# Kernel optimization log

Measured on AMD Instinct MI355X. Metric: run time of the kernel, lower is better.

## Reference

```python
import jax, jax.numpy as jnp
import numpy as np

EPS = 1e-5  # BatchNorm eps


def _add_self_loops(edge_index, num_nodes):
    loop = jnp.arange(num_nodes, dtype=edge_index.dtype)
    src = jnp.concatenate([edge_index[0], loop])
    dst = jnp.concatenate([edge_index[1], loop])
    return src, dst


def _gcn_conv(x, src, dst, norm, W, b, num_nodes):
    # PyG GCNConv: out = D^{-1/2} (A+I) D^{-1/2} (x W) + b
    h = x @ W                                # [N, out_dim]
    msg = h[src] * norm[:, None]             # [E+N, out_dim] gathered messages
    out = jax.ops.segment_sum(msg, dst, num_segments=num_nodes)
    return out + b


def _batch_norm(x, gamma, beta):
    # training-mode batch statistics over the node dimension (biased var)
    mean = jnp.mean(x, axis=0)
    var = jnp.var(x, axis=0)
    return (x - mean) * jax.lax.rsqrt(var + EPS) * gamma + beta


def setup_inputs() -> dict:
    key = jax.random.key(0)
    ks = jax.random.split(key, 10)
    N, E = 50000, 800000
    d_in, d_h, d_mid, d_out = 1536, 512, 128, 5

    x = jax.random.normal(ks[0], (N, d_in), dtype=jnp.float32)
    edge_index = jax.random.randint(ks[1], (2, E), 0, N, dtype=jnp.int32)

    def glorot(k, fan_in, fan_out):
        s = jnp.sqrt(6.0 / (fan_in + fan_out))
        return jax.random.uniform(k, (fan_in, fan_out), jnp.float32, -s, s)

    return {
        "x": x,
        "edge_index": edge_index,
        "W1": glorot(ks[2], d_in, d_h), "b1": jnp.zeros((d_h,), jnp.float32),
        "W2": glorot(ks[3], d_h, d_mid), "b2": jnp.zeros((d_mid,), jnp.float32),
        "W3": glorot(ks[4], d_mid, d_out), "b3": jnp.zeros((d_out,), jnp.float32),
        "gamma1": jnp.ones((d_h,), jnp.float32), "beta1": jnp.zeros((d_h,), jnp.float32),
        "gamma2": jnp.ones((d_mid,), jnp.float32), "beta2": jnp.zeros((d_mid,), jnp.float32),
    }


def reference(x, edge_index, W1, b1, W2, b2, W3, b3, gamma1, beta1, gamma2, beta2):
    N = x.shape[0]
    src, dst = _add_self_loops(edge_index, N)
    # symmetric degree normalization deg^{-1/2}[src] * deg^{-1/2}[dst]
    deg = jax.ops.segment_sum(jnp.ones_like(dst, dtype=x.dtype), dst, num_segments=N)
    inv_sqrt = jnp.where(deg > 0, jax.lax.rsqrt(deg), 0.0)
    norm = inv_sqrt[src] * inv_sqrt[dst]

    h = _gcn_conv(x, src, dst, norm, W1, b1, N)
    h = jax.nn.relu(_batch_norm(h, gamma1, beta1))  # dropout is identity in eval
    h = _gcn_conv(h, src, dst, norm, W2, b2, N)
    h = jax.nn.relu(_batch_norm(h, gamma2, beta2))
    h = _gcn_conv(h, src, dst, norm, W3, b3, N)
    return jax.nn.log_softmax(h, axis=1)
```

## Files before the change

### kernel.cpp

```cpp
#include <hip/hip_runtime.h>
#include <cstddef>
#include <cstdint>

typedef short s16x8 __attribute__((ext_vector_type(8)));
typedef unsigned short u16x4 __attribute__((ext_vector_type(4)));
typedef unsigned short u16x8 __attribute__((ext_vector_type(8)));
typedef float f32x4 __attribute__((ext_vector_type(4)));

__device__ __forceinline__ unsigned short f2bf(float f) {
  unsigned int u = __float_as_uint(f);
  u = (u + 0x7fffu + ((u >> 16) & 1u)) >> 16;
  return (unsigned short)u;
}
__device__ __forceinline__ float bf2f(unsigned short u) {
  return __uint_as_float(((unsigned int)u) << 16);
}

__device__ __forceinline__ void gl2lds16(const unsigned short* g, unsigned short* l) {
  __builtin_amdgcn_global_load_lds(
      (const __attribute__((address_space(1))) unsigned int*)g,
      (__attribute__((address_space(3))) unsigned int*)l, 16, 0, 0);
}

static inline size_t alignup(size_t x) { return (x + 255) & ~(size_t)255; }

__global__ void cvt_bf16_kernel(const float* __restrict__ in, unsigned short* __restrict__ out,
                                long n8) {
  long stride = (long)gridDim.x * blockDim.x;
  const float4* in4 = reinterpret_cast<const float4*>(in);
  u16x8* out8 = reinterpret_cast<u16x8*>(out);
  for (long i = blockIdx.x * (long)blockDim.x + threadIdx.x; i < n8; i += stride) {
    float4 a = in4[2 * i], b = in4[2 * i + 1];
    u16x8 p;
    p[0] = f2bf(a.x); p[1] = f2bf(a.y); p[2] = f2bf(a.z); p[3] = f2bf(a.w);
    p[4] = f2bf(b.x); p[5] = f2bf(b.y); p[6] = f2bf(b.z); p[7] = f2bf(b.w);
    out8[i] = p;
  }
}

__global__ void count_kernel(const int* __restrict__ dst, int* __restrict__ counts, int E) {
  int e = blockIdx.x * blockDim.x + threadIdx.x;
  if (e < E) atomicAdd(&counts[dst[e]], 1);
}

__global__ void invsqrt_kernel(const int* __restrict__ counts, float* __restrict__ inv_s, int n) {
  int i = blockIdx.x * blockDim.x + threadIdx.x;
  if (i < n) inv_s[i] = rsqrtf((float)(counts[i] + 1));
}

__global__ void block_sum_kernel(const int* __restrict__ counts, int* __restrict__ bsum, int n) {
  __shared__ int red[256];
  int i = blockIdx.x * 256 + threadIdx.x;
  red[threadIdx.x] = (i < n) ? counts[i] : 0;
  __syncthreads();
  #pragma unroll
  for (int o = 128; o > 0; o >>= 1) {
    if (threadIdx.x < o) red[threadIdx.x] += red[threadIdx.x + o];
    __syncthreads();
  }
  if (threadIdx.x == 0) bsum[blockIdx.x] = red[0];
}

__global__ void scan_bsum_kernel(int* __restrict__ bsum, int nb) {
  __shared__ int s[256];
  int t = threadIdx.x;
  s[t] = (t < nb) ? bsum[t] : 0;
  __syncthreads();
  #pragma unroll
  for (int o = 1; o < 256; o <<= 1) {
    int v = (t >= o) ? s[t - o] : 0;
    __syncthreads();
    s[t] += v;
    __syncthreads();
  }
  if (t < nb) bsum[t] = (t == 0) ? 0 : s[t - 1];
}

__global__ void scan_apply_kernel(const int* __restrict__ counts, const int* __restrict__ bpre,
                                  int* __restrict__ offsets, int n) {
  __shared__ int s[256];
  int t = threadIdx.x;
  int i = blockIdx.x * 256 + t;
  s[t] = (i < n) ? counts[i] : 0;
  __syncthreads();
  #pragma unroll
  for (int o = 1; o < 256; o <<= 1) {
    int v = (t >= o) ? s[t - o] : 0;
    __syncthreads();
    s[t] += v;
    __syncthreads();
  }
  if (i < n) offsets[i + 1] = s[t] + bpre[blockIdx.x];
  if (i == 0) offsets[0] = 0;
}

__global__ void fill_kernel(const int* __restrict__ src, const int* __restrict__ dst,
                            const int* __restrict__ offsets, int* __restrict__ cursor,
                            int* __restrict__ csr_src, int E) {
  int e = blockIdx.x * blockDim.x + threadIdx.x;
  if (e >= E) return;
  int d = dst[e];
  int pos = atomicAdd(&cursor[d], 1);
  csr_src[offsets[d] + pos] = src[e];
}

__global__ void transpose_w_kernel(const float* __restrict__ W, unsigned short* __restrict__ Wt,
                                   int K, int N) {
  __shared__ float tile[32][33];
  int k0 = blockIdx.x * 32, n0 = blockIdx.y * 32;
  int tx = threadIdx.x & 31, ty = threadIdx.x >> 5;
  #pragma unroll
  for (int i = 0; i < 32; i += 8)
    tile[ty + i][tx] = W[(size_t)(k0 + ty + i) * N + n0 + tx];
  __syncthreads();
  #pragma unroll
  for (int i = 0; i < 32; i += 8)
    Wt[(size_t)(n0 + ty + i) * K + k0 + tx] = f2bf(tile[tx][ty + i]);
}

__global__ __launch_bounds__(256) void gemm1_kernel(
    const unsigned short* __restrict__ A, const unsigned short* __restrict__ B,
    unsigned short* __restrict__ C, int M) {
  __shared__ __align__(16) unsigned short As[128 * 64];
  __shared__ __align__(16) unsigned short Bs[128 * 64];
  const int K = 1536;
  int tid = threadIdx.x, lane = tid & 63, w = tid >> 6;

  int nwg = gridDim.x * gridDim.y;
  int orig = blockIdx.y * gridDim.x + blockIdx.x;
  int q = nwg >> 3, r = nwg & 7;
  int xcd = orig & 7, loc = orig >> 3;
  int wg = (xcd < r) ? xcd * (q + 1) + loc : r * (q + 1) + (xcd - r) * q + loc;
  int bx = wg & 3, by = wg >> 2;

  int m0 = by * 128, n0 = bx * 128;
  int wm = (w >> 1) * 64, wn = (w & 1) * 64;

  f32x4 acc[4][4];
  #pragma unroll
  for (int i = 0; i < 4; i++)
    #pragma unroll
    for (int j = 0; j < 4; j++) acc[i][j] = (f32x4){0.f, 0.f, 0.f, 0.f};

  int srow[4], sgc[4];
  #pragma unroll
  for (int i = 0; i < 4; i++) {
    int s = i * 256 + tid;
    int row = s >> 3, j = s & 7;
    srow[i] = row;
    sgc[i] = (j ^ (row & 7)) << 3;
  }

  for (int k0 = 0; k0 < K; k0 += 64) {
    #pragma unroll
    for (int i = 0; i < 4; i++) {
      int s = i * 256 + tid;
      gl2lds16(&A[(size_t)(m0 + srow[i]) * K + k0 + sgc[i]], &As[s * 8]);
      gl2lds16(&B[(size_t)(n0 + srow[i]) * K + k0 + sgc[i]], &Bs[s * 8]);
    }
    __syncthreads();
    #pragma unroll
    for (int ks = 0; ks < 2; ks++) {
      s16x8 af[4], bfr[4];
      int jc = ks * 4 + (lane >> 4);
      #pragma unroll
      for (int i = 0; i < 4; i++) {
        int rr = wm + i * 16 + (lane & 15);
        af[i] = *reinterpret_cast<const s16x8*>(&As[rr * 64 + ((jc ^ (rr & 7)) << 3)]);
        int rn = wn + i * 16 + (lane & 15);
        bfr[i] = *reinterpret_cast<const s16x8*>(&Bs[rn * 64 + ((jc ^ (rn & 7)) << 3)]);
      }
      #pragma unroll
      for (int i = 0; i < 4; i++)
        #pragma unroll
        for (int j = 0; j < 4; j++)
          acc[i][j] = __builtin_amdgcn_mfma_f32_16x16x32_bf16(af[i], bfr[j], acc[i][j], 0, 0, 0);
    }
    __syncthreads();
  }
  #pragma unroll
  for (int i = 0; i < 4; i++) {
    #pragma unroll
    for (int j = 0; j < 4; j++) {
      int col = n0 + wn + j * 16 + (lane & 15);
      #pragma unroll
      for (int r2 = 0; r2 < 4; r2++) {
        int row = m0 + wm + i * 16 + (lane >> 4) * 4 + r2;
        if (row < M) C[(size_t)row * 512 + col] = f2bf(acc[i][j][r2]);
      }
    }
  }
}

#define LDT 72
__global__ __launch_bounds__(256) void gemm2_kernel(
    const unsigned short* __restrict__ A, const unsigned short* __restrict__ Bt,
    const float* __restrict__ sc, const float* __restrict__ sh,
    unsigned short* __restrict__ C, int M) {
  const int N = 128, K = 512;
  __shared__ unsigned short As[128 * LDT];
  __shared__ unsigned short Bs[128 * LDT];
  int tid = threadIdx.x;
  int m0 = blockIdx.y * 128;
  int w = tid >> 6, lane = tid & 63;
  int wm = (w >> 1) * 64, wn = (w & 1) * 64;

  f32x4 acc[4][4];
  #pragma unroll
  for (int i = 0; i < 4; i++)
    #pragma unroll
    for (int j = 0; j < 4; j++) acc[i][j] = (f32x4){0.f, 0.f, 0.f, 0.f};

  for (int k0 = 0; k0 < K; k0 += 64) {
    #pragma unroll
    for (int r = 0; r < 4; r++) {
      int idx = r * 256 + tid;
      int row = idx >> 3;
      int seg = (idx & 7) * 8;
      int gr = m0 + row;
      u16x8 v = (u16x8){0, 0, 0, 0, 0, 0, 0, 0};
      if (gr < M) v = *reinterpret_cast<const u16x8*>(&A[(size_t)gr * K + k0 + seg]);
      int c = k0 + seg;
      u16x8 p;
      #pragma unroll
      for (int j = 0; j < 8; j++) {
        float f = fmaxf(bf2f(v[j]) * sc[c + j] + sh[c + j], 0.f);
        p[j] = f2bf(f);
      }
      *reinterpret_cast<u16x8*>(&As[row * LDT + seg]) = p;
    }
    #pragma unroll
    for (int r = 0; r < 4; r++) {
      int idx = r * 256 + tid;
      int n = idx >> 3;
      int seg = (idx & 7) * 8;
      u16x8 v = *reinterpret_cast<const u16x8*>(&Bt[(size_t)n * K + k0 + seg]);
      *reinterpret_cast<u16x8*>(&Bs[n * LDT + seg]) = v;
    }
    __syncthreads();
    #pragma unroll
    for (int ks = 0; ks < 2; ks++) {
      s16x8 af[4], bfr[4];
      #pragma unroll
      for (int i = 0; i < 4; i++) {
        af[i]  = *reinterpret_cast<const s16x8*>(&As[(wm + i * 16 + (lane & 15)) * LDT + ks * 32 + (lane >> 4) * 8]);
        bfr[i] = *reinterpret_cast<const s16x8*>(&Bs[(wn + i * 16 + (lane & 15)) * LDT + ks * 32 + (lane >> 4) * 8]);
      }
      #pragma unroll
      for (int i = 0; i < 4; i++)
        #pragma unroll
        for (int j = 0; j < 4; j++)
          acc[i][j] = __builtin_amdgcn_mfma_f32_16x16x32_bf16(af[i], bfr[j], acc[i][j], 0, 0, 0);
    }
    __syncthreads();
  }
  #pragma unroll
  for (int i = 0; i < 4; i++) {
    #pragma unroll
    for (int j = 0; j < 4; j++) {
      int col = wn + j * 16 + (lane & 15);
      #pragma unroll
      for (int r = 0; r < 4; r++) {
        int row = m0 + wm + i * 16 + (lane >> 4) * 4 + r;
        if (row < M) C[(size_t)row * N + col] = f2bf(acc[i][j][r]);
      }
    }
  }
}

__global__ void agg512_kernel(const unsigned short* __restrict__ h, const int* __restrict__ offsets,
                              const int* __restrict__ csr, const float* __restrict__ inv_s,
                              unsigned short* __restrict__ out, int n) {
  int wv = threadIdx.x >> 6, lane = threadIdx.x & 63;
  int node = blockIdx.x * 4 + wv;
  if (node >= n) return;
  const u16x8* h8 = reinterpret_cast<const u16x8*>(h);
  float di = inv_s[node];
  size_t rb = (size_t)node * 64;
  float acc[8];
  u16x8 v0 = h8[rb + lane];
  float dd = di * di;
  #pragma unroll
  for (int j = 0; j < 8; j++) acc[j] = bf2f(v0[j]) * dd;
  int e = offsets[node], e1 = offsets[node + 1];
  for (; e + 1 < e1; e += 2) {
    int sA = csr[e], sB = csr[e + 1];
    float wA = inv_s[sA] * di, wB = inv_s[sB] * di;
    u16x8 vA = h8[(size_t)sA * 64 + lane];
    u16x8 vB = h8[(size_t)sB * 64 + lane];
    #pragma unroll
    for (int j = 0; j < 8; j++) acc[j] += bf2f(vA[j]) * wA + bf2f(vB[j]) * wB;
  }
  if (e < e1) {
    int sA = csr[e];
    float wA = inv_s[sA] * di;
    u16x8 vA = h8[(size_t)sA * 64 + lane];
    #pragma unroll
    for (int j = 0; j < 8; j++) acc[j] += bf2f(vA[j]) * wA;
  }
  u16x8 o;
  #pragma unroll
  for (int j = 0; j < 8; j++) o[j] = f2bf(acc[j]);
  reinterpret_cast<u16x8*>(out)[rb + lane] = o;
}

__global__ void agg128_kernel(const unsigned short* __restrict__ h, const int* __restrict__ offsets,
                              const int* __restrict__ csr, const float* __restrict__ inv_s,
                              unsigned short* __restrict__ out, int n) {
  int wv = threadIdx.x >> 6, lane = threadIdx.x & 63;
  int node = blockIdx.x * 4 + wv;
  if (node >= n) return;
  const unsigned int* h2 = reinterpret_cast<const unsigned int*>(h);
  float di = inv_s[node];
  size_t rb = (size_t)node * 64;
  unsigned int u0 = h2[rb + lane];
  float dd = di * di;
  float alo = __uint_as_float(u0 << 16) * dd;
  float ahi = __uint_as_float(u0 & 0xffff0000u) * dd;
  int e = offsets[node], e1 = offsets[node + 1];
  for (; e + 1 < e1; e += 2) {
    int sA = csr[e], sB = csr[e + 1];
    float wA = inv_s[sA] * di, wB = inv_s[sB] * di;
    unsigned int uA = h2[(size_t)sA * 64 + lane];
    unsigned int uB = h2[(size_t)sB * 64 + lane];
    alo += __uint_as_float(uA << 16) * wA + __uint_as_float(uB << 16) * wB;
    ahi += __uint_as_float(uA & 0xffff0000u) * wA + __uint_as_float(uB & 0xffff0000u) * wB;
  }
  if (e < e1) {
    int sA = csr[e];
    float wA = inv_s[sA] * di;
    unsigned int uA = h2[(size_t)sA * 64 + lane];
    alo += __uint_as_float(uA << 16) * wA;
    ahi += __uint_as_float(uA & 0xffff0000u) * wA;
  }
  unsigned int uo = ((unsigned int)f2bf(ahi) << 16) | (unsigned int)f2bf(alo);
  reinterpret_cast<unsigned int*>(out)[rb + lane] = uo;
}

__global__ void bn_stats512_kernel(const unsigned short* __restrict__ x, float* __restrict__ accum,
                                   int nrows, int rpb) {
  int r0 = blockIdx.x * rpb, r1 = min(nrows, r0 + rpb);
  int t = threadIdx.x;
  const unsigned int* x2 = reinterpret_cast<const unsigned int*>(x);
  float s0 = 0.f, q0 = 0.f, s1 = 0.f, q1 = 0.f;
  for (int r = r0; r < r1; r++) {
    unsigned int u = x2[(size_t)r * 256 + t];
    float lo = __uint_as_float(u << 16);
    float hi = __uint_as_float(u & 0xffff0000u);
    s0 += lo; q0 += lo * lo; s1 += hi; q1 += hi * hi;
  }
  atomicAdd(&accum[2 * t], s0);
  atomicAdd(&accum[2 * t + 1], s1);
  atomicAdd(&accum[512 + 2 * t], q0);
  atomicAdd(&accum[512 + 2 * t + 1], q1);
}

__global__ void bn_stats128_kernel(const unsigned short* __restrict__ x, float* __restrict__ accum,
                                   int nrows, int rpb) {
  int r0 = blockIdx.x * rpb, r1 = min(nrows, r0 + rpb);
  int t = threadIdx.x;
  int colu = t & 63, rofs = t >> 6;
  const unsigned int* x2 = reinterpret_cast<const unsigned int*>(x);
  float s0 = 0.f, q0 = 0.f, s1 = 0.f, q1 = 0.f;
  for (int r = r0 + rofs; r < r1; r += 4) {
    unsigned int u = x2[(size_t)r * 64 + colu];
    float lo = __uint_as_float(u << 16);
    float hi = __uint_as_float(u & 0xffff0000u);
    s0 += lo; q0 += lo * lo; s1 += hi; q1 += hi * hi;
  }
  atomicAdd(&accum[2 * colu], s0);
  atomicAdd(&accum[2 * colu + 1], s1);
  atomicAdd(&accum[128 + 2 * colu], q0);
  atomicAdd(&accum[128 + 2 * colu + 1], q1);
}

__global__ void bn_finalize_kernel(const float* __restrict__ accum, const float* __restrict__ gamma,
                                   const float* __restrict__ beta, float* __restrict__ scale,
                                   float* __restrict__ shift, int D, float invN) {
  int c = blockIdx.x * blockDim.x + threadIdx.x;
  if (c >= D) return;
  float mean = accum[c] * invN;
  float var = accum[D + c] * invN - mean * mean;
  float sc = gamma[c] * rsqrtf(var + 1e-5f);
  scale[c] = sc;
  shift[c] = beta[c] - mean * sc;
}

__global__ void gemm3_kernel(const unsigned short* __restrict__ A, const float* __restrict__ W,
                             const float* __restrict__ sc, const float* __restrict__ sh,
                             float* __restrict__ C, int M) {
  __shared__ float Ws[128 * 5];
  __shared__ float scs[128], shs[128];
  int tid = threadIdx.x;
  for (int i = tid; i < 128 * 5; i += blockDim.x) Ws[i] = W[i];
  if (tid < 128) { scs[tid] = sc[tid]; shs[tid] = sh[tid]; }
  __syncthreads();
  int row = blockIdx.x * blockDim.x + tid;
  if (row >= M) return;
  float acc[5] = {0.f, 0.f, 0.f, 0.f, 0.f};
  const u16x8* a8 = reinterpret_cast<const u16x8*>(A + (size_t)row * 128);
  for (int k8 = 0; k8 < 16; k8++) {
    u16x8 v = a8[k8];
    int k = k8 * 8;
    #pragma unroll
    for (int j = 0; j < 8; j++) {
      float f = fmaxf(bf2f(v[j]) * scs[k + j] + shs[k + j], 0.f);
      #pragma unroll
      for (int c = 0; c < 5; c++) acc[c] += f * Ws[(k + j) * 5 + c];
    }
  }
  #pragma unroll
  for (int j = 0; j < 5; j++) C[(size_t)row * 5 + j] = acc[j];
}

__global__ void agg3_lsm_kernel(const float* __restrict__ h, const int* __restrict__ offsets,
                                const int* __restrict__ csr, const float* __restrict__ inv_s,
                                const float* __restrict__ b3, float* __restrict__ out, int n) {
  int node = blockIdx.x * blockDim.x + threadIdx.x;
  if (node >= n) return;
  float di = inv_s[node];
  float acc[5];
  #pragma unroll
  for (int j = 0; j < 5; j++) acc[j] = h[(size_t)node * 5 + j] * di * di;
  int s0 = offsets[node], s1 = offsets[node + 1];
  for (int e = s0; e < s1; e++) {
    int s = csr[e];
    float wgt = inv_s[s] * di;
    #pragma unroll
    for (int j = 0; j < 5; j++) acc[j] += h[(size_t)s * 5 + j] * wgt;
  }
  #pragma unroll
  for (int j = 0; j < 5; j++) acc[j] += b3[j];
  float m = acc[0];
  #pragma unroll
  for (int j = 1; j < 5; j++) m = fmaxf(m, acc[j]);
  float sum = 0.f;
  #pragma unroll
  for (int j = 0; j < 5; j++) sum += expf(acc[j] - m);
  float lse = logf(sum);
  #pragma unroll
  for (int j = 0; j < 5; j++) out[(size_t)node * 5 + j] = acc[j] - m - lse;
}

extern "C" void kernel_launch(void* const* d_in, const int* in_sizes, int n_in,
                              void* d_out, int out_size, void* d_ws, size_t ws_size,
                              hipStream_t stream) {
  const float* x      = (const float*)d_in[0];
  const int*   ei     = (const int*)d_in[1];
  const float* W1     = (const float*)d_in[2];
  const float* b3     = (const float*)d_in[7];
  const float* W2     = (const float*)d_in[4];
  const float* W3     = (const float*)d_in[6];
  const float* gamma1 = (const float*)d_in[8];
  const float* beta1  = (const float*)d_in[9];
  const float* gamma2 = (const float*)d_in[10];
  const float* beta2  = (const float*)d_in[11];

  const int N = in_sizes[0] / 1536;
  const int E = in_sizes[1] / 2;
  const int* src = ei;
  const int* dst = ei + E;

  const int mblocks = (N + 127) / 128;
  const int Mpad = mblocks * 128;
  const int nb = (N + 255) / 256;

  char* ws = (char*)d_ws;
  size_t szRA = alignup((size_t)N * 512 * sizeof(float));
  size_t szXB = alignup((size_t)Mpad * 1536 * sizeof(unsigned short));
  char* RAb = ws;
  unsigned short* XB = (unsigned short*)(ws + szRA);
  char* RBb = ws + szRA;
  char* sp = ws + szRA + szXB;
  int* counts   = (int*)sp;           sp += alignup((size_t)N * 4);
  int* cursor   = (int*)sp;           sp += alignup((size_t)N * 4);
  int* offsets  = (int*)sp;           sp += alignup((size_t)(N + 1) * 4);
  int* csr_src  = (int*)sp;           sp += alignup((size_t)E * 4);
  float* inv_s  = (float*)sp;         sp += alignup((size_t)N * 4);
  unsigned short* W1t = (unsigned short*)sp; sp += alignup((size_t)512 * 1536 * 2);
  unsigned short* W2t = (unsigned short*)sp; sp += alignup((size_t)128 * 512 * 2);
  float* accum  = (float*)sp;         sp += alignup(1024 * 4);
  float* sc1    = (float*)sp;         sp += alignup(512 * 4);
  float* sh1    = (float*)sp;         sp += alignup(512 * 4);
  float* sc2    = (float*)sp;         sp += alignup(128 * 4);
  float* sh2    = (float*)sp;         sp += alignup(128 * 4);
  int* bsum     = (int*)sp;           sp += alignup(256 * 4);

  unsigned short* H1  = (unsigned short*)RAb;
  unsigned short* G1  = (unsigned short*)RBb;
  unsigned short* H2  = (unsigned short*)RAb;
  unsigned short* G2  = (unsigned short*)RBb;
  float*          H3  = (float*)RAb;

  cvt_bf16_kernel<<<2048, 256, 0, stream>>>(x, XB, (long)N * 1536 / 8);
  hipMemsetAsync(XB + (size_t)N * 1536, 0, (size_t)(Mpad - N) * 1536 * 2, stream);

  hipMemsetAsync(counts, 0, (size_t)N * 4, stream);
  hipMemsetAsync(cursor, 0, (size_t)N * 4, stream);
  count_kernel<<<(E + 255) / 256, 256, 0, stream>>>(dst, counts, E);
  invsqrt_kernel<<<(N + 255) / 256, 256, 0, stream>>>(counts, inv_s, N);
  block_sum_kernel<<<nb, 256, 0, stream>>>(counts, bsum, N);
  scan_bsum_kernel<<<1, 256, 0, stream>>>(bsum, nb);
  scan_apply_kernel<<<nb, 256, 0, stream>>>(counts, bsum, offsets, N);
  fill_kernel<<<(E + 255) / 256, 256, 0, stream>>>(src, dst, offsets, cursor, csr_src, E);

  transpose_w_kernel<<<dim3(1536 / 32, 512 / 32), 256, 0, stream>>>(W1, W1t, 1536, 512);
  transpose_w_kernel<<<dim3(512 / 32, 128 / 32), 256, 0, stream>>>(W2, W2t, 512, 128);

  int aggblocks = (N + 3) / 4;
  int rpb = (N + 511) / 512;

  gemm1_kernel<<<dim3(4, mblocks), 256, 0, stream>>>(XB, W1t, H1, N);
  agg512_kernel<<<aggblocks, 256, 0, stream>>>(H1, offsets, csr_src, inv_s, G1, N);
  hipMemsetAsync(accum, 0, 1024 * 4, stream);
  bn_stats512_kernel<<<512, 256, 0, stream>>>(G1, accum, N, rpb);
  bn_finalize_kernel<<<2, 256, 0, stream>>>(accum, gamma1, beta1, sc1, sh1, 512, 1.0f / N);

  gemm2_kernel<<<dim3(1, mblocks), 256, 0, stream>>>(G1, W2t, sc1, sh1, H2, N);
  agg128_kernel<<<aggblocks, 256, 0, stream>>>(H2, offsets, csr_src, inv_s, G2, N);
  hipMemsetAsync(accum, 0, 1024 * 4, stream);
  bn_stats128_kernel<<<512, 256, 0, stream>>>(G2, accum, N, rpb);
  bn_finalize_kernel<<<1, 256, 0, stream>>>(accum, gamma2, beta2, sc2, sh2, 128, 1.0f / N);

  gemm3_kernel<<<(N + 255) / 256, 256, 0, stream>>>(G2, W3, sc2, sh2, H3, N);
  agg3_lsm_kernel<<<(N + 255) / 256, 256, 0, stream>>>(H3, offsets, csr_src, inv_s, b3,
                                                       (float*)d_out, N);
}
```

Baseline: 695.5 us.

## Fuse fp32-to-bf16 conversion of x into GEMM1 A-tile loading

Removes the separate conversion kernel and padding memset for x. GEMM1 now reads fp32 x directly, converts it to bf16 in registers with packed convert instructions, and stores it into swizzled LDS. Out-of-range rows are zero-filled. This avoids writing and rereading a bf16 copy of x, but GEMM1 now reads twice as many bytes for A. Those loads are synchronous register loads rather than async global-to-LDS copies, and since gridDim.x is 4, each A row is converted four times.

```diff
diff --git a/kernel.cpp b/kernel.cpp
--- a/kernel.cpp
+++ b/kernel.cpp
@@ -23,20 +23,6 @@
 }
 
 static inline size_t alignup(size_t x) { return (x + 255) & ~(size_t)255; }
-
-__global__ void cvt_bf16_kernel(const float* __restrict__ in, unsigned short* __restrict__ out,
-                                long n8) {
-  long stride = (long)gridDim.x * blockDim.x;
-  const float4* in4 = reinterpret_cast<const float4*>(in);
-  u16x8* out8 = reinterpret_cast<u16x8*>(out);
-  for (long i = blockIdx.x * (long)blockDim.x + threadIdx.x; i < n8; i += stride) {
-    float4 a = in4[2 * i], b = in4[2 * i + 1];
-    u16x8 p;
-    p[0] = f2bf(a.x); p[1] = f2bf(a.y); p[2] = f2bf(a.z); p[3] = f2bf(a.w);
-    p[4] = f2bf(b.x); p[5] = f2bf(b.y); p[6] = f2bf(b.z); p[7] = f2bf(b.w);
-    out8[i] = p;
-  }
-}
 
 __global__ void count_kernel(const int* __restrict__ dst, int* __restrict__ counts, int E) {
   int e = blockIdx.x * blockDim.x + threadIdx.x;
@@ -119,7 +105,7 @@
 }
 
 __global__ __launch_bounds__(256) void gemm1_kernel(
-    const unsigned short* __restrict__ A, const unsigned short* __restrict__ B,
+    const float* __restrict__ A, const unsigned short* __restrict__ B,
     unsigned short* __restrict__ C, int M) {
   __shared__ __align__(16) unsigned short As[128 * 64];
   __shared__ __align__(16) unsigned short Bs[128 * 64];
@@ -142,20 +128,38 @@
     #pragma unroll
     for (int j = 0; j < 4; j++) acc[i][j] = (f32x4){0.f, 0.f, 0.f, 0.f};
 
-  int srow[4], sgc[4];
+  int srow[4], sgc[4], adst[4];
+  const float* aptr[4];
+  bool aok[4];
   #pragma unroll
   for (int i = 0; i < 4; i++) {
     int s = i * 256 + tid;
     int row = s >> 3, j = s & 7;
     srow[i] = row;
     sgc[i] = (j ^ (row & 7)) << 3;
+    adst[i] = row * 64 + sgc[i];
+    aok[i] = (m0 + row) < M;
+    aptr[i] = A + (size_t)(m0 + row) * K + j * 8;
   }
 
   for (int k0 = 0; k0 < K; k0 += 64) {
     #pragma unroll
     for (int i = 0; i < 4; i++) {
+      f32x4 a0 = (f32x4){0.f, 0.f, 0.f, 0.f}, a1 = (f32x4){0.f, 0.f, 0.f, 0.f};
+      if (aok[i]) {
+        const f32x4* p = reinterpret_cast<const f32x4*>(aptr[i] + k0);
+        a0 = p[0];
+        a1 = p[1];
+      }
+      unsigned int r0, r1, r2, r3;
+      asm("v_cvt_pk_bf16_f32 %0, %1, %2" : "=v"(r0) : "v"(a0[0]), "v"(a0[1]));
+      asm("v_cvt_pk_bf16_f32 %0, %1, %2" : "=v"(r1) : "v"(a0[2]), "v"(a0[3]));
+      asm("v_cvt_pk_bf16_f32 %0, %1, %2" : "=v"(r2) : "v"(a1[0]), "v"(a1[1]));
+      asm("v_cvt_pk_bf16_f32 %0, %1, %2" : "=v"(r3) : "v"(a1[2]), "v"(a1[3]));
+      uint4 pk;
+      pk.x = r0; pk.y = r1; pk.z = r2; pk.w = r3;
+      *reinterpret_cast<uint4*>(&As[adst[i]]) = pk;
       int s = i * 256 + tid;
-      gl2lds16(&A[(size_t)(m0 + srow[i]) * K + k0 + sgc[i]], &As[s * 8]);
       gl2lds16(&B[(size_t)(n0 + srow[i]) * K + k0 + sgc[i]], &Bs[s * 8]);
     }
     __syncthreads();
@@ -462,14 +466,12 @@
   const int* dst = ei + E;
 
   const int mblocks = (N + 127) / 128;
-  const int Mpad = mblocks * 128;
   const int nb = (N + 255) / 256;
 
   char* ws = (char*)d_ws;
   size_t szRA = alignup((size_t)N * 512 * sizeof(float));
-  size_t szXB = alignup((size_t)Mpad * 1536 * sizeof(unsigned short));
+  size_t szXB = alignup((size_t)(mblocks * 128) * 1536 * sizeof(unsigned short));
   char* RAb = ws;
-  unsigned short* XB = (unsigned short*)(ws + szRA);
   char* RBb = ws + szRA;
   char* sp = ws + szRA + szXB;
   int* counts   = (int*)sp;           sp += alignup((size_t)N * 4);
@@ -492,9 +494,6 @@
   unsigned short* G2  = (unsigned short*)RBb;
   float*          H3  = (float*)RAb;
 
-  cvt_bf16_kernel<<<2048, 256, 0, stream>>>(x, XB, (long)N * 1536 / 8);
-  hipMemsetAsync(XB + (size_t)N * 1536, 0, (size_t)(Mpad - N) * 1536 * 2, stream);
-
   hipMemsetAsync(counts, 0, (size_t)N * 4, stream);
   hipMemsetAsync(cursor, 0, (size_t)N * 4, stream);
   count_kernel<<<(E + 255) / 256, 256, 0, stream>>>(dst, counts, E);
@@ -510,7 +509,7 @@
   int aggblocks = (N + 3) / 4;
   int rpb = (N + 511) / 512;
 
-  gemm1_kernel<<<dim3(4, mblocks), 256, 0, stream>>>(XB, W1t, H1, N);
+  gemm1_kernel<<<dim3(4, mblocks), 256, 0, stream>>>(x, W1t, H1, N);
   agg512_kernel<<<aggblocks, 256, 0, stream>>>(H1, offsets, csr_src, inv_s, G1, N);
   hipMemsetAsync(accum, 0, 1024 * 4, stream);
   bn_stats512_kernel<<<512, 256, 0, stream>>>(G1, accum, N, rpb);
```

Result: slower. 731.6 us (+5.2%).

## Double-buffer gemm1 LDS loads and widen tile to 128x256 with 512 threads

Applied to the files above, without the earlier changes.

The first GEMM now works on 128x256 output tiles with 8 waves instead of 128x128 with 4. The K step drops to 32, and the LDS buffers for A and B are double-buffered so the global-to-LDS load of the next slice overlaps the MFMA work on the current one. This removes one barrier per iteration, gives more reuse of each A tile, and halves the number of workgroups. The risks are fewer blocks for occupancy and more loop iterations, each issuing fewer MFMAs per barrier.

```diff
diff --git a/kernel.cpp b/kernel.cpp
--- a/kernel.cpp
+++ b/kernel.cpp
@@ -118,12 +118,13 @@
     Wt[(size_t)(n0 + ty + i) * K + k0 + tx] = f2bf(tile[tx][ty + i]);
 }
 
-__global__ __launch_bounds__(256) void gemm1_kernel(
+__global__ __launch_bounds__(512) void gemm1_kernel(
     const unsigned short* __restrict__ A, const unsigned short* __restrict__ B,
     unsigned short* __restrict__ C, int M) {
-  __shared__ __align__(16) unsigned short As[128 * 64];
-  __shared__ __align__(16) unsigned short Bs[128 * 64];
+  __shared__ __align__(16) unsigned short As[2][128 * 32];
+  __shared__ __align__(16) unsigned short Bs[2][256 * 32];
   const int K = 1536;
+  const int NT = 48;
   int tid = threadIdx.x, lane = tid & 63, w = tid >> 6;
 
   int nwg = gridDim.x * gridDim.y;
@@ -131,10 +132,10 @@
   int q = nwg >> 3, r = nwg & 7;
   int xcd = orig & 7, loc = orig >> 3;
   int wg = (xcd < r) ? xcd * (q + 1) + loc : r * (q + 1) + (xcd - r) * q + loc;
-  int bx = wg & 3, by = wg >> 2;
-
-  int m0 = by * 128, n0 = bx * 128;
-  int wm = (w >> 1) * 64, wn = (w & 1) * 64;
+  int bx = wg & 1, by = wg >> 1;
+
+  int m0 = by * 128, n0 = bx * 256;
+  int wm = (w >> 2) * 64, wn = (w & 3) * 64;
 
   f32x4 acc[4][4];
   #pragma unroll
@@ -142,42 +143,47 @@
     #pragma unroll
     for (int j = 0; j < 4; j++) acc[i][j] = (f32x4){0.f, 0.f, 0.f, 0.f};
 
-  int srow[4], sgc[4];
-  #pragma unroll
-  for (int i = 0; i < 4; i++) {
-    int s = i * 256 + tid;
-    int row = s >> 3, j = s & 7;
-    srow[i] = row;
-    sgc[i] = (j ^ (row & 7)) << 3;
-  }
-
-  for (int k0 = 0; k0 < K; k0 += 64) {
+  int arow = tid >> 2, aslot = tid & 3;
+  int asrc = (aslot ^ (arow & 3)) << 3;
+  const unsigned short* agp = &A[(size_t)(m0 + arow) * K + asrc];
+  int adst = tid * 8;
+  int brow = tid >> 2, bslot = tid & 3;
+  int bsrc = (bslot ^ (brow & 3)) << 3;
+  const unsigned short* bgp0 = &B[(size_t)(n0 + brow) * K + bsrc];
+  const unsigned short* bgp1 = &B[(size_t)(n0 + 128 + brow) * K + bsrc];
+  int bdst0 = tid * 8, bdst1 = (512 + tid) * 8;
+
+  gl2lds16(agp, &As[0][adst]);
+  gl2lds16(bgp0, &Bs[0][bdst0]);
+  gl2lds16(bgp1, &Bs[0][bdst1]);
+  __syncthreads();
+
+  int cur = 0;
+  for (int t = 0; t < NT; t++) {
+    if (t + 1 < NT) {
+      int kb = (t + 1) * 32;
+      gl2lds16(agp + kb, &As[cur ^ 1][adst]);
+      gl2lds16(bgp0 + kb, &Bs[cur ^ 1][bdst0]);
+      gl2lds16(bgp1 + kb, &Bs[cur ^ 1][bdst1]);
+    }
+    s16x8 af[4], bfr[4];
+    int jc = lane >> 4;
     #pragma unroll
     for (int i = 0; i < 4; i++) {
-      int s = i * 256 + tid;
-      gl2lds16(&A[(size_t)(m0 + srow[i]) * K + k0 + sgc[i]], &As[s * 8]);
-      gl2lds16(&B[(size_t)(n0 + srow[i]) * K + k0 + sgc[i]], &Bs[s * 8]);
-    }
-    __syncthreads();
-    #pragma unroll
-    for (int ks = 0; ks < 2; ks++) {
-      s16x8 af[4], bfr[4];
-      int jc = ks * 4 + (lane >> 4);
-      #pragma unroll
-      for (int i = 0; i < 4; i++) {
-        int rr = wm + i * 16 + (lane & 15);
-        af[i] = *reinterpret_cast<const s16x8*>(&As[rr * 64 + ((jc ^ (rr & 7)) << 3)]);
-        int rn = wn + i * 16 + (lane & 15);
-        bfr[i] = *reinterpret_cast<const s16x8*>(&Bs[rn * 64 + ((jc ^ (rn & 7)) << 3)]);
-      }
-      #pragma unroll
-      for (int i = 0; i < 4; i++)
-        #pragma unroll
-        for (int j = 0; j < 4; j++)
-          acc[i][j] = __builtin_amdgcn_mfma_f32_16x16x32_bf16(af[i], bfr[j], acc[i][j], 0, 0, 0);
-    }
-    __syncthreads();
-  }
+      int rr = wm + i * 16 + (lane & 15);
+      af[i] = *reinterpret_cast<const s16x8*>(&As[cur][rr * 32 + ((jc ^ (rr & 3)) << 3)]);
+      int rn = wn + i * 16 + (lane & 15);
+      bfr[i] = *reinterpret_cast<const s16x8*>(&Bs[cur][rn * 32 + ((jc ^ (rn & 3)) << 3)]);
+    }
+    #pragma unroll
+    for (int i = 0; i < 4; i++)
+      #pragma unroll
+      for (int j = 0; j < 4; j++)
+        acc[i][j] = __builtin_amdgcn_mfma_f32_16x16x32_bf16(af[i], bfr[j], acc[i][j], 0, 0, 0);
+    __syncthreads();
+    cur ^= 1;
+  }
+
   #pragma unroll
   for (int i = 0; i < 4; i++) {
     #pragma unroll
@@ -510,7 +516,7 @@
   int aggblocks = (N + 3) / 4;
   int rpb = (N + 511) / 512;
 
-  gemm1_kernel<<<dim3(4, mblocks), 256, 0, stream>>>(XB, W1t, H1, N);
+  gemm1_kernel<<<dim3(2, mblocks), 512, 0, stream>>>(XB, W1t, H1, N);
   agg512_kernel<<<aggblocks, 256, 0, stream>>>(H1, offsets, csr_src, inv_s, G1, N);
   hipMemsetAsync(accum, 0, 1024 * 4, stream);
   bn_stats512_kernel<<<512, 256, 0, stream>>>(G1, accum, N, rpb);
```

Result: no change. 697.1 us (+0.2%).
